# Kernel optimization log

Measured on AMD Instinct MI355X. Metric: run time of the kernel, lower is better.

## Reference

```python
import jax, jax.numpy as jnp
import numpy as np

N_ITER = 10
EPS = 1e-20
REG = 1e-6


def _nmf(Tn, Vn, Yn):
    # Tn [I,K], Vn [K,J], Yn [I,J] complex. T,V are strictly positive, so
    # torch's .abs() on Rn is the identity.
    Rn = Tn @ Vn
    Y_d_R = jnp.abs(Yn) ** 2 / (Rn ** 2 + EPS)
    Rn_d = 1.0 / (Rn + EPS)
    Tn = Tn * jnp.sqrt((Y_d_R @ Vn.T) / (Rn_d @ Vn.T + EPS))
    Vn = Vn * jnp.sqrt((Tn.T @ Y_d_R) / (Tn.T @ Rn_d + EPS))
    Rn_new = Tn @ Vn
    return Tn, Vn, Rn_new


def _forward(X, T0, V0):
    M, J, I, _ = X.shape
    N = M
    # [M,J,I,2] real -> [I,M,J] complex64
    X_c = (X[..., 0] + 1j * X[..., 1]).astype(jnp.complex64).transpose(2, 0, 1)
    eye = jnp.eye(M, dtype=jnp.complex64)
    W = jnp.broadcast_to(eye[None], (I, M, M)).astype(jnp.complex64) + jnp.zeros((I, M, M), jnp.complex64)
    Y = jnp.einsum('inm,imj->inj', W, X_c)  # [I,N,J]
    T = T0
    V = V0

    def body(carry, _):
        W, Y, T, V = carry
        for n in range(N):  # N == 2, structurally small static loop
            Tn, Vn, Rn = _nmf(T[:, :, n], V[:, :, n], Y[:, n, :])
            T = T.at[:, :, n].set(Tn)
            V = V.at[:, :, n].set(Vn)
            inv_sqrt_Rn = jnp.sqrt(1.0 / (Rn + EPS))  # [I,J] real
            Xw = X_c * inv_sqrt_Rn[:, None, :]  # [I,M,J] complex
            D = Xw @ jnp.conj(Xw).transpose(0, 2, 1) / J + REG * eye[None]  # [I,M,M]
            A = W @ D
            e_n = jnp.broadcast_to(eye[:, n][None, :, None], (D.shape[0], M, 1))
            b = jnp.linalg.solve(A, e_n)  # [I,M,1]
            bH = jnp.conj(b).transpose(0, 2, 1)
            denom = jnp.sqrt((bH @ D @ b).real + EPS)  # [I,1,1]
            w = jnp.conj((b / denom)[:, :, 0])  # [I,M]
            W = W.at[:, n, :].set(w)
        Y = jnp.einsum('inm,imj->inj', W, X_c)
        return (W, Y, T, V), None

    (W, Y, T, V), _ = jax.lax.scan(body, (W, Y, T, V), None, length=N_ITER)
    Y_out = Y.transpose(1, 2, 0)  # [N,J,I]
    return jnp.stack([Y_out.real, Y_out.imag], axis=-1)  # [N,J,I,2]


def setup_inputs() -> dict:
    key = jax.random.key(0)
    k1, k2, k3 = jax.random.split(key, 3)
    M, J, I, K = 2, 1024, 1025, 8
    X = jax.random.normal(k1, (M, J, I, 2), dtype=jnp.float32)
    T0 = jax.random.uniform(k2, (I, K, M), dtype=jnp.float32) * (1 - 1e-8) + 1e-8
    V0 = jax.random.uniform(k3, (K, J, M), dtype=jnp.float32) * (1 - 1e-8) + 1e-8
    return {"X": X, "T0": T0, "V0": V0}


def reference(X, T0, V0):
    return _forward(X, T0, V0)
```

## Files before the change

### kernel.cpp

```cpp
#include <hip/hip_runtime.h>
#include <math.h>

#define I_DIM 1025
#define J_DIM 1024
#define K_DIM 8
#define N_ITER 10
#define EPS 1e-20f
#define REG 1e-6f
#define MODE_CD  1
#define MODE_NMF 2

__device__ __forceinline__ float __frcp(float x){ return __builtin_amdgcn_rcpf(x); }

__device__ __forceinline__ float2 cmul(float2 a, float2 b){
  return make_float2(a.x*b.x - a.y*b.y, a.x*b.y + a.y*b.x);
}
__device__ __forceinline__ float2 cadd(float2 a, float2 b){
  return make_float2(a.x+b.x, a.y+b.y);
}
__device__ __forceinline__ float2 csub(float2 a, float2 b){
  return make_float2(a.x-b.x, a.y-b.y);
}
__device__ __forceinline__ float2 cconj(float2 a){ return make_float2(a.x, -a.y); }
__device__ __forceinline__ float2 cscale(float2 a, float s){ return make_float2(a.x*s, a.y*s); }
__device__ __forceinline__ float2 cdivc(float2 a, float2 d){
  float inv = 1.0f/(d.x*d.x + d.y*d.y);
  return make_float2((a.x*d.x + a.y*d.y)*inv, (a.y*d.x - a.x*d.y)*inv);
}

__global__ __launch_bounds__(256) void k_setup(
    const float2* __restrict__ X, const float* __restrict__ T0, const float* __restrict__ V0,
    float4* __restrict__ Xc4, float4* __restrict__ XcT,
    float* __restrict__ Tw, float* __restrict__ Vw, float2* __restrict__ Wm){
  __shared__ float4 tile[32][33];
  int b = blockIdx.x, tid = threadIdx.x;
  int gtid = b*256 + tid;
  if (gtid < 2*K_DIM*I_DIM){
    int i = gtid % I_DIM; int rest = gtid / I_DIM;
    int k = rest & 7, n = rest >> 3;
    Tw[gtid] = T0[(i*K_DIM+k)*2 + n];
  }
  if (gtid < 2*K_DIM*J_DIM){
    int n = gtid/(K_DIM*J_DIM), rem = gtid%(K_DIM*J_DIM);
    int k = rem/J_DIM, j = rem%J_DIM;
    Vw[gtid] = V0[(k*J_DIM+j)*2 + n];
  }
  if (gtid < I_DIM*4){
    int rc = gtid & 3;
    Wm[gtid] = make_float2((rc==0||rc==3)?1.0f:0.0f, 0.0f);
  }
  int ib = b / 32, jb = b % 32;
  int i0 = ib*32, j0 = jb*32;
  int tx = tid & 31, ty = tid >> 5;
  #pragma unroll
  for (int r=0;r<4;r++){
    int jl = ty + r*8; int i = i0 + tx;
    if (i < I_DIM){
      float2 a = X[(size_t)(0*J_DIM + j0 + jl)*I_DIM + i];
      float2 c = X[(size_t)(1*J_DIM + j0 + jl)*I_DIM + i];
      float4 val = make_float4(a.x, a.y, c.x, c.y);
      tile[jl][tx] = val;
      XcT[(size_t)(j0+jl)*I_DIM + i] = val;
    }
  }
  __syncthreads();
  #pragma unroll
  for (int r=0;r<4;r++){
    int il = ty + r*8; int i = i0 + il;
    if (i < I_DIM) Xc4[(size_t)i*J_DIM + j0 + tx] = tile[tx][il];
  }
}

template<int MODE>
__global__ __launch_bounds__(256) void k_cda(const float4* __restrict__ Xc4,
      float* __restrict__ Tw, float* __restrict__ Told, const float* __restrict__ Vw,
      float2* __restrict__ Wm){
  int i = blockIdx.x, tid = threadIdx.x;
  int n = tid >> 7, jl = tid & 127;
  __shared__ float redD[4][4];
  __shared__ float redT[4][16];
  __shared__ float wsh[8];

  float t[8];
  #pragma unroll
  for (int k=0;k<8;k++) t[k] = Tw[(size_t)(n*K_DIM+k)*I_DIM + i];

  const float* vb = Vw + (size_t)(n*K_DIM)*J_DIM + jl;
  float r_s[8] = {0,0,0,0,0,0,0,0};
  #pragma unroll
  for (int k=0;k<8;k++){
    #pragma unroll
    for (int s=0;s<8;s++) r_s[s] += t[k]*vb[k*J_DIM + 128*s];
  }
  float q_s[8];
  #pragma unroll
  for (int s=0;s<8;s++) q_s[s] = __frcp(r_s[s] + EPS);

  const float4* xb = Xc4 + (size_t)i*J_DIM + jl;
  float4 x_s[8];
  #pragma unroll
  for (int s=0;s<8;s++) x_s[s] = xb[128*s];

  if (MODE & MODE_CD){
    float d00=0.0f, d11=0.0f, dre=0.0f, dim_=0.0f;
    #pragma unroll
    for (int s=0;s<8;s++){
      float4 x = x_s[s]; float q = q_s[s];
      d00 += (x.x*x.x + x.y*x.y)*q;
      d11 += (x.z*x.z + x.w*x.w)*q;
      dre += (x.x*x.z + x.y*x.w)*q;
      dim_ += (x.y*x.z - x.x*x.w)*q;
    }
    #pragma unroll
    for (int off=32; off>0; off>>=1){
      d00 += __shfl_down(d00,off); d11 += __shfl_down(d11,off);
      dre += __shfl_down(dre,off); dim_ += __shfl_down(dim_,off);
    }
    {
      int lane = tid&63, wv = tid>>6;
      if (lane==0){ redD[wv][0]=d00; redD[wv][1]=d11; redD[wv][2]=dre; redD[wv][3]=dim_; }
    }
    __syncthreads();
    if (tid==0){
      const float invJ = 1.0f/(float)J_DIM;
      float D[2][4];
      #pragma unroll
      for (int c=0;c<4;c++){
        D[0][c] = (redD[0][c]+redD[1][c])*invJ;
        D[1][c] = (redD[2][c]+redD[3][c])*invJ;
      }
      float2 w00 = Wm[i*4+0], w01 = Wm[i*4+1], w10 = Wm[i*4+2], w11 = Wm[i*4+3];
      #pragma unroll
      for (int nn=0;nn<2;nn++){
        float d00_ = D[nn][0] + REG, d11_ = D[nn][1] + REG;
        float2 d01 = make_float2(D[nn][2], D[nn][3]);
        float2 d10 = cconj(d01);
        float2 A00 = cadd(cscale(w00, d00_), cmul(w01, d10));
        float2 A01 = cadd(cmul(w00, d01), cscale(w01, d11_));
        float2 A10 = cadd(cscale(w10, d00_), cmul(w11, d10));
        float2 A11 = cadd(cmul(w10, d01), cscale(w11, d11_));
        float2 det = csub(cmul(A00,A11), cmul(A01,A10));
        float2 bu0, bu1;
        if (nn==0){ bu0 = A11; bu1 = make_float2(-A10.x, -A10.y); }
        else      { bu0 = make_float2(-A01.x, -A01.y); bu1 = A00; }
        float2 b0 = cdivc(bu0, det);
        float2 b1 = cdivc(bu1, det);
        float quad = d00_*(b0.x*b0.x + b0.y*b0.y) + d11_*(b1.x*b1.x + b1.y*b1.y);
        float2 u = cmul(d01, b1);
        quad += 2.0f*(b0.x*u.x + b0.y*u.y);
        float inv = 1.0f/sqrtf(quad + EPS);
        float2 wn0 = make_float2(b0.x*inv, -b0.y*inv);
        float2 wn1 = make_float2(b1.x*inv, -b1.y*inv);
        if (nn==0){ w00=wn0; w01=wn1; } else { w10=wn0; w11=wn1; }
      }
      Wm[i*4+0]=w00; Wm[i*4+1]=w01; Wm[i*4+2]=w10; Wm[i*4+3]=w11;
      wsh[0]=w00.x; wsh[1]=w00.y; wsh[2]=w01.x; wsh[3]=w01.y;
      wsh[4]=w10.x; wsh[5]=w10.y; wsh[6]=w11.x; wsh[7]=w11.y;
    }
  } else {
    if (tid < 4){ float2 w = Wm[i*4+tid]; wsh[tid*2]=w.x; wsh[tid*2+1]=w.y; }
  }
  __syncthreads();
  if (!(MODE & MODE_NMF)) return;

  if ((tid & 127) < 8){
    int kk = tid & 7;
    Told[(size_t)(n*K_DIM+kk)*I_DIM + i] = t[kk];
  }

  float2 w0 = make_float2(wsh[n*4+0], wsh[n*4+1]);
  float2 w1 = make_float2(wsh[n*4+2], wsh[n*4+3]);
  float p_s[8];
  #pragma unroll
  for (int s=0;s<8;s++){
    float4 x = x_s[s];
    float yre = w0.x*x.x - w0.y*x.y + w1.x*x.z - w1.y*x.w;
    float yim = w0.x*x.y + w0.y*x.x + w1.x*x.w + w1.y*x.z;
    float q = q_s[s];
    p_s[s] = (yre*yre + yim*yim)*q*q;
  }
  float aN[8], aD[8];
  #pragma unroll
  for (int k=0;k<8;k++){
    float sn = 0.0f, sd = 0.0f;
    #pragma unroll
    for (int s=0;s<8;s++){
      float v = vb[k*J_DIM + 128*s];
      sn += p_s[s]*v; sd += q_s[s]*v;
    }
    aN[k] = sn; aD[k] = sd;
  }
  #pragma unroll
  for (int k=0;k<8;k++){
    #pragma unroll
    for (int off=32; off>0; off>>=1){
      aN[k] += __shfl_down(aN[k],off);
      aD[k] += __shfl_down(aD[k],off);
    }
  }
  {
    int lane = tid&63, wv = tid>>6;
    if (lane==0){
      #pragma unroll
      for (int k=0;k<8;k++){ redT[wv][k]=aN[k]; redT[wv][k+8]=aD[k]; }
    }
  }
  __syncthreads();
  if ((tid & 127) < 8){
    int kk = tid & 7;
    int wb = (tid>>7)*2;
    float ns = redT[wb][kk]   + redT[wb+1][kk];
    float ds = redT[wb][kk+8] + redT[wb+1][kk+8];
    size_t ti = (size_t)(n*K_DIM+kk)*I_DIM + i;
    Tw[ti] = Tw[ti]*sqrtf(ns*__frcp(ds + EPS));
  }
}

__global__ __launch_bounds__(256) void k_vupd(const float4* __restrict__ XcT,
      const float* __restrict__ Tw, const float* __restrict__ Told,
      float* __restrict__ Vw, const float2* __restrict__ Wm){
  int n = blockIdx.y;
  int tid = threadIdx.x;
  int jj = tid & 3, ii = tid >> 2;
  int j = blockIdx.x*4 + jj;
  float v[8];
  #pragma unroll
  for (int k=0;k<8;k++) v[k] = Vw[(size_t)(n*K_DIM+k)*J_DIM + j];
  float aN[8] = {0,0,0,0,0,0,0,0};
  float aD[8] = {0,0,0,0,0,0,0,0};
  const float* tob = Told + (size_t)(n*K_DIM)*I_DIM;
  const float* tnb = Tw   + (size_t)(n*K_DIM)*I_DIM;
  const float4* xcb = XcT + (size_t)j*I_DIM;
  #pragma unroll 2
  for (int i=ii; i<I_DIM; i+=64){
    float to[8], tn[8];
    #pragma unroll
    for (int k=0;k<8;k++){ to[k] = tob[k*I_DIM + i]; tn[k] = tnb[k*I_DIM + i]; }
    float4 wv = *(const float4*)&Wm[i*4 + n*2];
    float4 x  = xcb[i];
    float r = to[0]*v[0]+to[1]*v[1]+to[2]*v[2]+to[3]*v[3]
            + to[4]*v[4]+to[5]*v[5]+to[6]*v[6]+to[7]*v[7];
    float yre = wv.x*x.x - wv.y*x.y + wv.z*x.z - wv.w*x.w;
    float yim = wv.x*x.y + wv.y*x.x + wv.z*x.w + wv.w*x.z;
    float q = __frcp(r + EPS);
    float p = (yre*yre + yim*yim)*q*q;
    #pragma unroll
    for (int k=0;k<8;k++){ aN[k] += tn[k]*p; aD[k] += tn[k]*q; }
  }
  #pragma unroll
  for (int k=0;k<8;k++){
    #pragma unroll
    for (int off=32; off>=4; off>>=1){
      aN[k] += __shfl_down(aN[k],off);
      aD[k] += __shfl_down(aD[k],off);
    }
  }
  __shared__ float red[4][4][16];
  int wv_ = tid>>6, lane = tid&63;
  if (lane < 4){
    #pragma unroll
    for (int k=0;k<8;k++){ red[wv_][lane][k]=aN[k]; red[wv_][lane][k+8]=aD[k]; }
  }
  __syncthreads();
  if (tid < 32){
    int jj2 = tid>>3, k = tid&7;
    float num = red[0][jj2][k]+red[1][jj2][k]+red[2][jj2][k]+red[3][jj2][k];
    float den = red[0][jj2][k+8]+red[1][jj2][k+8]+red[2][jj2][k+8]+red[3][jj2][k+8];
    size_t vi = (size_t)(n*K_DIM+k)*J_DIM + blockIdx.x*4 + jj2;
    Vw[vi] *= sqrtf(num*__frcp(den + EPS));
  }
}

__global__ void k_final(const float4* __restrict__ Xc4, const float2* __restrict__ Wm,
                        float2* __restrict__ out){
  __shared__ float2 yt[2][32][33];
  int i0 = blockIdx.x*32, j0 = blockIdx.y*32;
  int tx = threadIdx.x, ty = threadIdx.y;
  int j = j0 + tx;
  #pragma unroll
  for (int r=0;r<4;r++){
    int il = ty + r*8; int i = i0 + il;
    if (i < I_DIM){
      float4 x = Xc4[(size_t)i*J_DIM + j];
      #pragma unroll
      for (int n=0;n<2;n++){
        float2 a = Wm[i*4+n*2+0], b = Wm[i*4+n*2+1];
        float2 y;
        y.x = a.x*x.x - a.y*x.y + b.x*x.z - b.y*x.w;
        y.y = a.x*x.y + a.y*x.x + b.x*x.w + b.y*x.z;
        yt[n][tx][il] = y;
      }
    }
  }
  __syncthreads();
  int i = i0 + tx;
  if (i < I_DIM){
    #pragma unroll
    for (int n=0;n<2;n++){
      #pragma unroll
      for (int r=0;r<4;r++){
        int jl = ty + r*8;
        out[(size_t)(n*J_DIM + j0 + jl)*I_DIM + i] = yt[n][jl][tx];
      }
    }
  }
}

extern "C" void kernel_launch(void* const* d_in, const int* in_sizes, int n_in,
                              void* d_out, int out_size, void* d_ws, size_t ws_size,
                              hipStream_t stream){
  const float2* X  = (const float2*)d_in[0];
  const float*  T0 = (const float*)d_in[1];
  const float*  V0 = (const float*)d_in[2];

  char* ws = (char*)d_ws;
  size_t off = 0;
  auto alloc = [&](size_t bytes)->char*{
    char* p = ws + off; off += (bytes + 255) & ~(size_t)255; return p;
  };
  float4* Xc4  = (float4*)alloc((size_t)I_DIM*J_DIM*sizeof(float4));
  float4* XcT  = (float4*)alloc((size_t)J_DIM*I_DIM*sizeof(float4));
  float*  Tw   = (float*) alloc((size_t)2*K_DIM*I_DIM*sizeof(float));
  float*  Told = (float*) alloc((size_t)2*K_DIM*I_DIM*sizeof(float));
  float*  Vw   = (float*) alloc((size_t)2*K_DIM*J_DIM*sizeof(float));
  float2* Wm   = (float2*)alloc((size_t)I_DIM*4*sizeof(float2));

  k_setup<<<33*32, 256, 0, stream>>>(X, T0, V0, Xc4, XcT, Tw, Vw, Wm);
  k_cda<MODE_NMF><<<I_DIM, 256, 0, stream>>>(Xc4, Tw, Told, Vw, Wm);
  for (int it=0; it<N_ITER; it++){
    k_vupd<<<dim3(J_DIM/4, 2), 256, 0, stream>>>(XcT, Tw, Told, Vw, Wm);
    if (it < N_ITER-1)
      k_cda<MODE_CD|MODE_NMF><<<I_DIM, 256, 0, stream>>>(Xc4, Tw, Told, Vw, Wm);
    else
      k_cda<MODE_CD><<<I_DIM, 256, 0, stream>>>(Xc4, Tw, Told, Vw, Wm);
  }
  k_final<<<dim3(33,32), dim3(32,8), 0, stream>>>(Xc4, Wm, (float2*)d_out);
}
```

Baseline: 305.5 us.

## Interleave old/new T, store V k-contiguous, use shared atomics for reductions

T old and new values are packed into one float2 array, so k_vupd reads both with one load per k and k_cda no longer writes a separate Told buffer. V is stored j-major with its 8 k-values contiguous, so each j's factors load as two float4s in both kernels. Cross-lane shuffle reductions are replaced by shared-memory float atomics, and k_vupd's thread mapping changes so that each wave handles one j. The atomics may serialize heavily, since every thread of a block hits the same few shared addresses, and they make the summation order nondeterministic.

Result: slower. 764.7 us (+150.3%).

```diff
diff --git a/kernel.cpp b/kernel.cpp
--- a/kernel.cpp
+++ b/kernel.cpp
@@ -31,18 +31,19 @@
 __global__ __launch_bounds__(256) void k_setup(
     const float2* __restrict__ X, const float* __restrict__ T0, const float* __restrict__ V0,
     float4* __restrict__ Xc4, float4* __restrict__ XcT,
-    float* __restrict__ Tw, float* __restrict__ Vw, float2* __restrict__ Wm){
+    float2* __restrict__ Tp, float* __restrict__ Vw, float2* __restrict__ Wm){
   __shared__ float4 tile[32][33];
   int b = blockIdx.x, tid = threadIdx.x;
   int gtid = b*256 + tid;
   if (gtid < 2*K_DIM*I_DIM){
     int i = gtid % I_DIM; int rest = gtid / I_DIM;
     int k = rest & 7, n = rest >> 3;
-    Tw[gtid] = T0[(i*K_DIM+k)*2 + n];
+    float t0 = T0[(i*K_DIM+k)*2 + n];
+    Tp[gtid] = make_float2(t0, t0);
   }
   if (gtid < 2*K_DIM*J_DIM){
-    int n = gtid/(K_DIM*J_DIM), rem = gtid%(K_DIM*J_DIM);
-    int k = rem/J_DIM, j = rem%J_DIM;
+    int n = gtid >> 13, rem = gtid & 8191;
+    int j = rem >> 3, k = rem & 7;
     Vw[gtid] = V0[(k*J_DIM+j)*2 + n];
   }
   if (gtid < I_DIM*4){
@@ -73,29 +74,36 @@
 
 template<int MODE>
 __global__ __launch_bounds__(256) void k_cda(const float4* __restrict__ Xc4,
-      float* __restrict__ Tw, float* __restrict__ Told, const float* __restrict__ Vw,
+      float2* __restrict__ Tp, const float4* __restrict__ Vw4,
       float2* __restrict__ Wm){
   int i = blockIdx.x, tid = threadIdx.x;
   int n = tid >> 7, jl = tid & 127;
-  __shared__ float redD[4][4];
-  __shared__ float redT[4][16];
+  __shared__ float dsh[8];
+  __shared__ float ash[32];
   __shared__ float wsh[8];
+  if (tid < 8)  dsh[tid] = 0.0f;
+  if (tid < 32) ash[tid] = 0.0f;
+  __syncthreads();
 
   float t[8];
-  #pragma unroll
-  for (int k=0;k<8;k++) t[k] = Tw[(size_t)(n*K_DIM+k)*I_DIM + i];
-
-  const float* vb = Vw + (size_t)(n*K_DIM)*J_DIM + jl;
-  float r_s[8] = {0,0,0,0,0,0,0,0};
-  #pragma unroll
-  for (int k=0;k<8;k++){
-    #pragma unroll
-    for (int s=0;s<8;s++) r_s[s] += t[k]*vb[k*J_DIM + 128*s];
-  }
-  float q_s[8];
-  #pragma unroll
-  for (int s=0;s<8;s++) q_s[s] = __frcp(r_s[s] + EPS);
-
+  {
+    const float2* tb = Tp + (size_t)n*K_DIM*I_DIM + i;
+    #pragma unroll
+    for (int k=0;k<8;k++) t[k] = tb[(size_t)k*I_DIM].y;
+  }
+
+  const float4* vbase = Vw4 + ((size_t)n*J_DIM)*2;
+  float r_s[8], q_s[8];
+  #pragma unroll
+  for (int s=0;s<8;s++){
+    int j = jl + 128*s;
+    float4 va = vbase[(size_t)j*2 + 0];
+    float4 vb = vbase[(size_t)j*2 + 1];
+    float r = t[0]*va.x + t[1]*va.y + t[2]*va.z + t[3]*va.w
+            + t[4]*vb.x + t[5]*vb.y + t[6]*vb.z + t[7]*vb.w;
+    r_s[s] = r;
+    q_s[s] = __frcp(r + EPS);
+  }
   const float4* xb = Xc4 + (size_t)i*J_DIM + jl;
   float4 x_s[8];
   #pragma unroll
@@ -111,24 +119,18 @@
       dre += (x.x*x.z + x.y*x.w)*q;
       dim_ += (x.y*x.z - x.x*x.w)*q;
     }
-    #pragma unroll
-    for (int off=32; off>0; off>>=1){
-      d00 += __shfl_down(d00,off); d11 += __shfl_down(d11,off);
-      dre += __shfl_down(dre,off); dim_ += __shfl_down(dim_,off);
-    }
-    {
-      int lane = tid&63, wv = tid>>6;
-      if (lane==0){ redD[wv][0]=d00; redD[wv][1]=d11; redD[wv][2]=dre; redD[wv][3]=dim_; }
-    }
+    atomicAdd(&dsh[n*4+0], d00);
+    atomicAdd(&dsh[n*4+1], d11);
+    atomicAdd(&dsh[n*4+2], dre);
+    atomicAdd(&dsh[n*4+3], dim_);
     __syncthreads();
     if (tid==0){
       const float invJ = 1.0f/(float)J_DIM;
       float D[2][4];
       #pragma unroll
-      for (int c=0;c<4;c++){
-        D[0][c] = (redD[0][c]+redD[1][c])*invJ;
-        D[1][c] = (redD[2][c]+redD[3][c])*invJ;
-      }
+      for (int nn=0;nn<2;nn++)
+        #pragma unroll
+        for (int c=0;c<4;c++) D[nn][c] = dsh[nn*4+c]*invJ;
       float2 w00 = Wm[i*4+0], w01 = Wm[i*4+1], w10 = Wm[i*4+2], w11 = Wm[i*4+3];
       #pragma unroll
       for (int nn=0;nn<2;nn++){
@@ -163,11 +165,6 @@
   __syncthreads();
   if (!(MODE & MODE_NMF)) return;
 
-  if ((tid & 127) < 8){
-    int kk = tid & 7;
-    Told[(size_t)(n*K_DIM+kk)*I_DIM + i] = t[kk];
-  }
-
   float2 w0 = make_float2(wsh[n*4+0], wsh[n*4+1]);
   float2 w1 = make_float2(wsh[n*4+2], wsh[n*4+3]);
   float p_s[8];
@@ -179,94 +176,75 @@
     float q = q_s[s];
     p_s[s] = (yre*yre + yim*yim)*q*q;
   }
-  float aN[8], aD[8];
+  float aN[8] = {0,0,0,0,0,0,0,0};
+  float aD[8] = {0,0,0,0,0,0,0,0};
+  #pragma unroll
+  for (int s=0;s<8;s++){
+    int j = jl + 128*s;
+    float4 va = vbase[(size_t)j*2 + 0];
+    float4 vb = vbase[(size_t)j*2 + 1];
+    float p = p_s[s], q = q_s[s];
+    aN[0]+=p*va.x; aN[1]+=p*va.y; aN[2]+=p*va.z; aN[3]+=p*va.w;
+    aN[4]+=p*vb.x; aN[5]+=p*vb.y; aN[6]+=p*vb.z; aN[7]+=p*vb.w;
+    aD[0]+=q*va.x; aD[1]+=q*va.y; aD[2]+=q*va.z; aD[3]+=q*va.w;
+    aD[4]+=q*vb.x; aD[5]+=q*vb.y; aD[6]+=q*vb.z; aD[7]+=q*vb.w;
+  }
   #pragma unroll
   for (int k=0;k<8;k++){
-    float sn = 0.0f, sd = 0.0f;
-    #pragma unroll
-    for (int s=0;s<8;s++){
-      float v = vb[k*J_DIM + 128*s];
-      sn += p_s[s]*v; sd += q_s[s]*v;
-    }
-    aN[k] = sn; aD[k] = sd;
-  }
-  #pragma unroll
-  for (int k=0;k<8;k++){
-    #pragma unroll
-    for (int off=32; off>0; off>>=1){
-      aN[k] += __shfl_down(aN[k],off);
-      aD[k] += __shfl_down(aD[k],off);
-    }
-  }
-  {
-    int lane = tid&63, wv = tid>>6;
-    if (lane==0){
-      #pragma unroll
-      for (int k=0;k<8;k++){ redT[wv][k]=aN[k]; redT[wv][k+8]=aD[k]; }
-    }
+    atomicAdd(&ash[n*16+k],   aN[k]);
+    atomicAdd(&ash[n*16+8+k], aD[k]);
   }
   __syncthreads();
   if ((tid & 127) < 8){
     int kk = tid & 7;
-    int wb = (tid>>7)*2;
-    float ns = redT[wb][kk]   + redT[wb+1][kk];
-    float ds = redT[wb][kk+8] + redT[wb+1][kk+8];
-    size_t ti = (size_t)(n*K_DIM+kk)*I_DIM + i;
-    Tw[ti] = Tw[ti]*sqrtf(ns*__frcp(ds + EPS));
+    float ns = ash[n*16+kk], ds = ash[n*16+8+kk];
+    float tn = t[kk]*sqrtf(ns*__frcp(ds + EPS));
+    Tp[(size_t)(n*K_DIM+kk)*I_DIM + i] = make_float2(t[kk], tn);
   }
 }
 
 __global__ __launch_bounds__(256) void k_vupd(const float4* __restrict__ XcT,
-      const float* __restrict__ Tw, const float* __restrict__ Told,
-      float* __restrict__ Vw, const float2* __restrict__ Wm){
+      const float2* __restrict__ Tp, float* __restrict__ Vw,
+      const float2* __restrict__ Wm){
   int n = blockIdx.y;
   int tid = threadIdx.x;
-  int jj = tid & 3, ii = tid >> 2;
+  int jj = tid >> 6, ii = tid & 63;
   int j = blockIdx.x*4 + jj;
-  float v[8];
-  #pragma unroll
-  for (int k=0;k<8;k++) v[k] = Vw[(size_t)(n*K_DIM+k)*J_DIM + j];
+  __shared__ float red[4][16];
+  if (tid < 64) ((float*)red)[tid] = 0.0f;
+  __syncthreads();
+
+  const float4* vj = (const float4*)(Vw + ((size_t)n*J_DIM + j)*8);
+  float4 va = vj[0], vb = vj[1];
   float aN[8] = {0,0,0,0,0,0,0,0};
   float aD[8] = {0,0,0,0,0,0,0,0};
-  const float* tob = Told + (size_t)(n*K_DIM)*I_DIM;
-  const float* tnb = Tw   + (size_t)(n*K_DIM)*I_DIM;
+  const float2* tb = Tp + (size_t)n*K_DIM*I_DIM;
   const float4* xcb = XcT + (size_t)j*I_DIM;
-  #pragma unroll 2
   for (int i=ii; i<I_DIM; i+=64){
-    float to[8], tn[8];
-    #pragma unroll
-    for (int k=0;k<8;k++){ to[k] = tob[k*I_DIM + i]; tn[k] = tnb[k*I_DIM + i]; }
+    float2 tp[8];
+    #pragma unroll
+    for (int k=0;k<8;k++) tp[k] = tb[(size_t)k*I_DIM + i];
     float4 wv = *(const float4*)&Wm[i*4 + n*2];
     float4 x  = xcb[i];
-    float r = to[0]*v[0]+to[1]*v[1]+to[2]*v[2]+to[3]*v[3]
-            + to[4]*v[4]+to[5]*v[5]+to[6]*v[6]+to[7]*v[7];
+    float r = tp[0].x*va.x + tp[1].x*va.y + tp[2].x*va.z + tp[3].x*va.w
+            + tp[4].x*vb.x + tp[5].x*vb.y + tp[6].x*vb.z + tp[7].x*vb.w;
     float yre = wv.x*x.x - wv.y*x.y + wv.z*x.z - wv.w*x.w;
     float yim = wv.x*x.y + wv.y*x.x + wv.z*x.w + wv.w*x.z;
     float q = __frcp(r + EPS);
     float p = (yre*yre + yim*yim)*q*q;
     #pragma unroll
-    for (int k=0;k<8;k++){ aN[k] += tn[k]*p; aD[k] += tn[k]*q; }
+    for (int k=0;k<8;k++){ aN[k] += tp[k].y*p; aD[k] += tp[k].y*q; }
   }
   #pragma unroll
   for (int k=0;k<8;k++){
-    #pragma unroll
-    for (int off=32; off>=4; off>>=1){
-      aN[k] += __shfl_down(aN[k],off);
-      aD[k] += __shfl_down(aD[k],off);
-    }
-  }
-  __shared__ float red[4][4][16];
-  int wv_ = tid>>6, lane = tid&63;
-  if (lane < 4){
-    #pragma unroll
-    for (int k=0;k<8;k++){ red[wv_][lane][k]=aN[k]; red[wv_][lane][k+8]=aD[k]; }
+    atomicAdd(&red[jj][k],   aN[k]);
+    atomicAdd(&red[jj][k+8], aD[k]);
   }
   __syncthreads();
   if (tid < 32){
     int jj2 = tid>>3, k = tid&7;
-    float num = red[0][jj2][k]+red[1][jj2][k]+red[2][jj2][k]+red[3][jj2][k];
-    float den = red[0][jj2][k+8]+red[1][jj2][k+8]+red[2][jj2][k+8]+red[3][jj2][k+8];
-    size_t vi = (size_t)(n*K_DIM+k)*J_DIM + blockIdx.x*4 + jj2;
+    float num = red[jj2][k], den = red[jj2][k+8];
+    size_t vi = ((size_t)n*J_DIM + blockIdx.x*4 + jj2)*8 + k;
     Vw[vi] *= sqrtf(num*__frcp(den + EPS));
   }
 }
@@ -320,19 +298,18 @@
   };
   float4* Xc4  = (float4*)alloc((size_t)I_DIM*J_DIM*sizeof(float4));
   float4* XcT  = (float4*)alloc((size_t)J_DIM*I_DIM*sizeof(float4));
-  float*  Tw   = (float*) alloc((size_t)2*K_DIM*I_DIM*sizeof(float));
-  float*  Told = (float*) alloc((size_t)2*K_DIM*I_DIM*sizeof(float));
-  float*  Vw   = (float*) alloc((size_t)2*K_DIM*J_DIM*sizeof(float));
+  float2* Tp   = (float2*)alloc((size_t)2*K_DIM*I_DIM*sizeof(float2));
+  float*  Vw   = (float*) alloc((size_t)2*J_DIM*K_DIM*sizeof(float));
   float2* Wm   = (float2*)alloc((size_t)I_DIM*4*sizeof(float2));
 
-  k_setup<<<33*32, 256, 0, stream>>>(X, T0, V0, Xc4, XcT, Tw, Vw, Wm);
-  k_cda<MODE_NMF><<<I_DIM, 256, 0, stream>>>(Xc4, Tw, Told, Vw, Wm);
+  k_setup<<<33*32, 256, 0, stream>>>(X, T0, V0, Xc4, XcT, Tp, Vw, Wm);
+  k_cda<MODE_NMF><<<I_DIM, 256, 0, stream>>>(Xc4, Tp, (const float4*)Vw, Wm);
   for (int it=0; it<N_ITER; it++){
-    k_vupd<<<dim3(J_DIM/4, 2), 256, 0, stream>>>(XcT, Tw, Told, Vw, Wm);
+    k_vupd<<<dim3(J_DIM/4, 2), 256, 0, stream>>>(XcT, Tp, Vw, Wm);
     if (it < N_ITER-1)
-      k_cda<MODE_CD|MODE_NMF><<<I_DIM, 256, 0, stream>>>(Xc4, Tw, Told, Vw, Wm);
+      k_cda<MODE_CD|MODE_NMF><<<I_DIM, 256, 0, stream>>>(Xc4, Tp, (const float4*)Vw, Wm);
     else
-      k_cda<MODE_CD><<<I_DIM, 256, 0, stream>>>(Xc4, Tw, Told, Vw, Wm);
+      k_cda<MODE_CD><<<I_DIM, 256, 0, stream>>>(Xc4, Tp, (const float4*)Vw, Wm);
   }
   k_final<<<dim3(33,32), dim3(32,8), 0, stream>>>(Xc4, Wm, (float2*)d_out);
 }
```
